# Kernel tuning notes

Measured on AMD Instinct MI355X. Metric: run time of the kernel, lower is better.

The kernel has to match this reference:

```python
import jax, jax.numpy as jnp
import numpy as np

H_IMG, W_IMG = 32, 32   # image_size -> seq_len = 1024
NH, HD, D = 8, 32, 256  # num_heads, head_dim, d_model
B = 8


def _relative_positions(h, w):
    # Swin-style relative position index table, [h*w, h*w] int32
    y = np.arange(h); x = np.arange(w)
    coords = np.stack(np.meshgrid(y, x, indexing='ij')).reshape(2, -1)  # [2, S]
    rel = coords[:, :, None] - coords[:, None, :]                      # [2, S, S]
    rel = rel.transpose(1, 2, 0).astype(np.int64)                      # [S, S, 2]
    rel[:, :, 0] += h - 1
    rel[:, :, 1] += w - 1
    rel[:, :, 0] *= 2 * w - 1
    return np.int32(rel.sum(-1))                                       # [S, S]

_POS = _relative_positions(H_IMG, W_IMG)


def setup_inputs() -> dict:
    key = jax.random.key(0)
    ks = jax.random.split(key, 8)
    S = H_IMG * W_IMG
    return {
        'inputs_q': jax.random.normal(ks[0], (B, S, D), jnp.float32),
        'inputs_kv': jax.random.normal(ks[1], (B, S, D), jnp.float32),
        'Wq': jax.random.normal(ks[2], (D, NH, HD), jnp.float32) / np.sqrt(D),
        'bq': jnp.zeros((NH, HD), jnp.float32),
        'Wk': jax.random.normal(ks[3], (D, NH, HD), jnp.float32) / np.sqrt(D),
        'bk': jnp.zeros((NH, HD), jnp.float32),
        'Wv': jax.random.normal(ks[4], (D, NH, HD), jnp.float32) / np.sqrt(D),
        'bv': jnp.zeros((NH, HD), jnp.float32),
        'rel_table': 0.02 * jax.random.normal(ks[5], ((2 * H_IMG - 1) * (2 * W_IMG - 1), NH), jnp.float32),
        'Wo': jax.random.normal(ks[6], (NH, HD, D), jnp.float32) / np.sqrt(NH * HD),
        'bo': jnp.zeros((D,), jnp.float32),
    }


def reference(inputs_q, inputs_kv, Wq, bq, Wk, bk, Wv, bv, rel_table, Wo, bo):
    pos = jnp.asarray(_POS)                                  # [S, S] int32 (constant)
    q = jnp.einsum('bsd,dhk->bshk', inputs_q, Wq) + bq       # [B, S, H, HD]
    k = jnp.einsum('bsd,dhk->bshk', inputs_kv, Wk) + bk
    v = jnp.einsum('bsd,dhk->bshk', inputs_kv, Wv) + bv
    q = q / jnp.sqrt(jnp.asarray(HD, q.dtype))
    attn = jnp.einsum('bqhd,bkhd->bhqk', q, k)               # [B, H, S, S]
    rel_bias = rel_table[pos]                                # [S, S, H]
    attn = attn + jnp.transpose(rel_bias, (2, 0, 1))[None]   # broadcast over batch
    attn = jax.nn.softmax(attn, axis=-1)
    x = jnp.einsum('bhqk,bkhd->bqhd', attn, v)               # [B, S, H, HD]
    return jnp.einsum('bqhd,hdf->bqf', x, Wo) + bo           # [B, S, D]
```

## Files before the change

### kernel.cpp

```cpp
#include <hip/hip_runtime.h>

#define B_SZ   8
#define S_LEN  1024
#define D_MOD  256
#define NHEADS 8
#define M_ROWS 8192
#define LOG2E  1.4426950408889634f
#define QSCALE_LOG2E 0.2550352766751165f

typedef _Float16 f16x8 __attribute__((ext_vector_type(8)));
typedef _Float16 f16x4 __attribute__((ext_vector_type(4)));
typedef float    f32x4 __attribute__((ext_vector_type(4)));

__global__ __launch_bounds__(256)
void prep_kernel(const float* __restrict__ Wq, const float* __restrict__ Wk,
                 const float* __restrict__ Wv, const float* __restrict__ Wo,
                 const float* __restrict__ rel,
                 _Float16* __restrict__ wtp, _Float16* __restrict__ tab) {
    if (blockIdx.x < 32) {
        __shared__ _Float16 Wl[32 * 264];
        const int mi = blockIdx.x >> 3;
        const int k0 = (blockIdx.x & 7) << 5;
        const float* W = (mi == 0) ? Wq : (mi == 1) ? Wk : (mi == 2) ? Wv : Wo;
        {
            const int r  = threadIdx.x >> 3;
            const int c4 = (threadIdx.x & 7) * 4;
            const float* src = W + (size_t)(k0 + r) * 256 + c4;
#pragma unroll
            for (int g = 0; g < 8; ++g) {
                f32x4 v = *(const f32x4*)(src + g * 32);
                f16x4 o;
#pragma unroll
                for (int j = 0; j < 4; ++j) o[j] = (_Float16)v[j];
                *(f16x4*)(&Wl[r * 264 + c4 + g * 32]) = o;
            }
        }
        __syncthreads();
        const int n16 = threadIdx.x >> 4;
        const int l16 = threadIdx.x & 15;
        const int kk  = k0 >> 5;
#pragma unroll
        for (int quad = 0; quad < 4; ++quad) {
            f16x8 v;
#pragma unroll
            for (int j = 0; j < 8; ++j) v[j] = Wl[(quad * 8 + j) * 264 + n16 * 16 + l16];
            *(f16x8*)(wtp + (((size_t)(mi * 16 + n16) * 8 + kk) << 9) + (quad * 16 + l16) * 8) = v;
        }
        return;
    }
    __shared__ float rl[63 * 8];
    const int dy31 = blockIdx.x - 32;
    for (int f = threadIdx.x; f < 504; f += 256) rl[f] = rel[(size_t)dy31 * 504 + f];
    __syncthreads();
    const int h  = threadIdx.x >> 5;
    const int r5 = threadIdx.x & 31;
#pragma unroll
    for (int c = 0; c < 6; ++c) {
        const int oi   = r5 * 6 + c;
        const int e    = oi >> 6;
        const int lane = oi & 63;
        const int quad = lane >> 4, l16 = lane & 15;
        f16x4 v;
#pragma unroll
        for (int reg = 0; reg < 4; ++reg) {
            const int idx = 16 * e + l16 - quad * 4 - reg + 15;
            v[reg] = (_Float16)(rl[idx * 8 + h] * LOG2E);
        }
        *(f16x4*)(tab + (((size_t)(h * 63 + dy31) * 3 + e) << 8) + lane * 4) = v;
    }
}

__global__ __launch_bounds__(256)
void gemm_qkv_kernel(const float* __restrict__ in_q, const float* __restrict__ in_kv,
                     const _Float16* __restrict__ wtp,
                     const float* __restrict__ bq, const float* __restrict__ bk,
                     const float* __restrict__ bv,
                     _Float16* __restrict__ qs, _Float16* __restrict__ ks,
                     _Float16* __restrict__ vs) {
    __shared__ __align__(16) _Float16 As[64 * 264];
    _Float16* Ta = As;
    _Float16* Tb = As + 64 * 72;

    const int tid  = threadIdx.x;
    const int w    = tid >> 6;
    const int lane = tid & 63;
    const int quad = lane >> 4;
    const int l16  = lane & 15;
    const int m0 = blockIdx.x * 64, n0 = blockIdx.y * 64, z = blockIdx.z;
    const int b = m0 >> 10, mloc = m0 & 1023;

    {
        const int r  = tid >> 2;
        const int c4 = (tid & 3) * 4;
        const float* src = (z ? in_kv : in_q) + (size_t)(m0 + r) * 256 + c4;
        _Float16* dst = As + r * 264 + c4;
#pragma unroll
        for (int g = 0; g < 16; ++g) {
            f32x4 v = *(const f32x4*)(src + g * 16);
            f16x4 o;
#pragma unroll
            for (int j = 0; j < 4; ++j) o[j] = (_Float16)v[j];
            *(f16x4*)(dst + g * 16) = o;
        }
    }
    __syncthreads();

    const int n16base = (n0 >> 4) + (w >> 1) * 2;
    const int mA = z ? 1 : 0;
    const _Float16* wA0 = wtp + (((size_t)(mA * 16 + n16base + 0) * 8) << 9) + lane * 8;
    const _Float16* wA1 = wtp + (((size_t)(mA * 16 + n16base + 1) * 8) << 9) + lane * 8;
    const _Float16* wV0 = wtp + (((size_t)(2 * 16 + n16base + 0) * 8) << 9) + lane * 8;
    const _Float16* wV1 = wtp + (((size_t)(2 * 16 + n16base + 1) * 8) << 9) + lane * 8;
    const _Float16* arow0 = As + ((w & 1) * 32 + l16) * 264;
    const _Float16* arow1 = arow0 + 16 * 264;

    f32x4 accA[2][2], accV[2][2];
#pragma unroll
    for (int i = 0; i < 2; ++i)
#pragma unroll
        for (int j = 0; j < 2; ++j) {
            accA[i][j] = (f32x4){0.f, 0.f, 0.f, 0.f};
            accV[i][j] = (f32x4){0.f, 0.f, 0.f, 0.f};
        }

#pragma unroll
    for (int kk = 0; kk < 8; ++kk) {
        const int k8 = kk * 32 + quad * 8;
        f16x8 a0 = *(const f16x8*)(arow0 + k8);
        f16x8 a1 = *(const f16x8*)(arow1 + k8);
        f16x8 w0 = *(const f16x8*)(wA0 + kk * 512);
        f16x8 w1 = *(const f16x8*)(wA1 + kk * 512);
        accA[0][0] = __builtin_amdgcn_mfma_f32_16x16x32_f16(w0, a0, accA[0][0], 0, 0, 0);
        accA[0][1] = __builtin_amdgcn_mfma_f32_16x16x32_f16(w0, a1, accA[0][1], 0, 0, 0);
        accA[1][0] = __builtin_amdgcn_mfma_f32_16x16x32_f16(w1, a0, accA[1][0], 0, 0, 0);
        accA[1][1] = __builtin_amdgcn_mfma_f32_16x16x32_f16(w1, a1, accA[1][1], 0, 0, 0);
        if (z == 1) {
            f16x8 v0 = *(const f16x8*)(wV0 + kk * 512);
            f16x8 v1 = *(const f16x8*)(wV1 + kk * 512);
            accV[0][0] = __builtin_amdgcn_mfma_f32_16x16x32_f16(a0, v0, accV[0][0], 0, 0, 0);
            accV[0][1] = __builtin_amdgcn_mfma_f32_16x16x32_f16(a0, v1, accV[0][1], 0, 0, 0);
            accV[1][0] = __builtin_amdgcn_mfma_f32_16x16x32_f16(a1, v0, accV[1][0], 0, 0, 0);
            accV[1][1] = __builtin_amdgcn_mfma_f32_16x16x32_f16(a1, v1, accV[1][1], 0, 0, 0);
        }
    }
    __syncthreads();

    {
        const float* biasA = z ? bk : bq;
        const float  sc    = z ? 1.0f : QSCALE_LOG2E;
#pragma unroll
        for (int i = 0; i < 2; ++i) {
            f32x4 b4 = *(const f32x4*)(biasA + n0 + (w >> 1) * 32 + i * 16 + quad * 4);
#pragma unroll
            for (int jj = 0; jj < 2; ++jj) {
                f16x4 pk;
#pragma unroll
                for (int r = 0; r < 4; ++r) pk[r] = (_Float16)((accA[i][jj][r] + b4[r]) * sc);
                *(f16x4*)(Ta + ((w & 1) * 32 + jj * 16 + l16) * 72 +
                               (w >> 1) * 32 + i * 16 + quad * 4) = pk;
            }
        }
        if (z == 1) {
#pragma unroll
            for (int i = 0; i < 2; ++i) {
                const float bvv = bv[n0 + (w >> 1) * 32 + i * 16 + l16];
#pragma unroll
                for (int jj = 0; jj < 2; ++jj) {
                    f16x4 pk;
#pragma unroll
                    for (int r = 0; r < 4; ++r) pk[r] = (_Float16)(accV[jj][i][r] + bvv);
                    *(f16x4*)(Tb + ((w >> 1) * 32 + i * 16 + l16) * 72 +
                                   (w & 1) * 32 + jj * 16 + quad * 4) = pk;
                }
            }
        }
    }
    __syncthreads();
    {
        const int l16c = tid & 15, qdc = (tid >> 4) & 3;
        const int tile0 = mloc >> 5;
#pragma unroll
        for (int c2i = 0; c2i < 2; ++c2i) {
            const int c2 = w * 2 + c2i;
            const int s2 = c2 >> 2, sub = (c2 >> 1) & 1, hs = c2 & 1;
            const int bh = b * 8 + (n0 >> 5) + hs;
            const size_t dbase = (((size_t)(bh * 32 + tile0 + s2) * 2 + sub) << 9) + lane * 8;
            f16x8 va = *(const f16x8*)(Ta + (s2 * 32 + sub * 16 + l16c) * 72 +
                                            hs * 32 + qdc * 8);
            *(f16x8*)((z ? ks : qs) + dbase) = va;
            if (z == 1) {
                f16x8 vb = *(const f16x8*)(Tb + (hs * 32 + sub * 16 + l16c) * 72 +
                                                s2 * 32 + qdc * 8);
                *(f16x8*)(vs + dbase) = vb;
            }
        }
    }
}

__global__ __launch_bounds__(256)
void gemm_out_kernel(const _Float16* __restrict__ xh, const _Float16* __restrict__ wtp,
                     const float* __restrict__ bo, float* __restrict__ out) {
    __shared__ __align__(16) _Float16 As[64 * 264];
    const int tid  = threadIdx.x;
    const int w    = tid >> 6;
    const int lane = tid & 63;
    const int quad = lane >> 4;
    const int l16  = lane & 15;
    const int m0 = blockIdx.x * 64, n0 = blockIdx.y * 64;

    {
        const int r  = tid >> 2;
        const int c8 = (tid & 3) * 8;
        const _Float16* src = xh + (size_t)(m0 + r) * 256 + c8;
        _Float16* dst = As + r * 264 + c8;
#pragma unroll
        for (int g = 0; g < 8; ++g)
            *(f16x8*)(dst + g * 32) = *(const f16x8*)(src + g * 32);
    }
    __syncthreads();

    const int n16base = 48 + (n0 >> 4) + (w >> 1) * 2;
    const _Float16* w0p = wtp + (((size_t)(n16base + 0) * 8) << 9) + lane * 8;
    const _Float16* w1p = wtp + (((size_t)(n16base + 1) * 8) << 9) + lane * 8;
    const _Float16* arow0 = As + ((w & 1) * 32 + l16) * 264;
    const _Float16* arow1 = arow0 + 16 * 264;

    f32x4 acc[2][2];
#pragma unroll
    for (int i = 0; i < 2; ++i)
#pragma unroll
        for (int j = 0; j < 2; ++j) acc[i][j] = (f32x4){0.f, 0.f, 0.f, 0.f};

#pragma unroll
    for (int kk = 0; kk < 8; ++kk) {
        const int k8 = kk * 32 + quad * 8;
        f16x8 a0 = *(const f16x8*)(arow0 + k8);
        f16x8 a1 = *(const f16x8*)(arow1 + k8);
        f16x8 b0 = *(const f16x8*)(w0p + kk * 512);
        f16x8 b1 = *(const f16x8*)(w1p + kk * 512);
        acc[0][0] = __builtin_amdgcn_mfma_f32_16x16x32_f16(a0, b0, acc[0][0], 0, 0, 0);
        acc[0][1] = __builtin_amdgcn_mfma_f32_16x16x32_f16(a0, b1, acc[0][1], 0, 0, 0);
        acc[1][0] = __builtin_amdgcn_mfma_f32_16x16x32_f16(a1, b0, acc[1][0], 0, 0, 0);
        acc[1][1] = __builtin_amdgcn_mfma_f32_16x16x32_f16(a1, b1, acc[1][1], 0, 0, 0);
    }

    __syncthreads();
    {
        float* Tf = (float*)As;
#pragma unroll
        for (int i = 0; i < 2; ++i) {
#pragma unroll
            for (int jj = 0; jj < 2; ++jj) {
#pragma unroll
                for (int r = 0; r < 4; ++r) {
                    const int row = (w & 1) * 32 + jj * 16 + quad * 4 + r;
                    const int col = (w >> 1) * 32 + i * 16 + l16;
                    Tf[row * 68 + col] = acc[jj][i][r];
                }
            }
        }
        __syncthreads();
        const f32x4 bv4 = *(const f32x4*)(bo + n0 + l16 * 4);
#pragma unroll
        for (int g = 0; g < 4; ++g) {
            const int row = w * 16 + g * 4 + quad;
            f32x4 v = *(const f32x4*)(Tf + row * 68 + l16 * 4);
            v += bv4;
            *(f32x4*)(out + (size_t)(m0 + row) * 256 + n0 + l16 * 4) = v;
        }
    }
}

__global__ __launch_bounds__(256)
void attn_kernel(const _Float16* __restrict__ qs, const _Float16* __restrict__ ks,
                 const _Float16* __restrict__ vs, const _Float16* __restrict__ tab,
                 _Float16* __restrict__ xh) {
    __shared__ __align__(16) _Float16 Ps[4][32][40];
    __shared__ __align__(16) _Float16 KVb[2][4][512];

    const int tid  = threadIdx.x;
    const int w    = tid >> 6;
    const int lane = tid & 63;
    const int quad = lane >> 4;
    const int l16  = lane & 15;

    const int n     = blockIdx.x;
    const int xcd   = n & 7;
    const int local = n >> 3;
    const int bh    = xcd * 8 + (local & 7);
    const int qc    = local >> 3;
    const int b = bh >> 3, h = bh & 7;
    const int qrow_base = qc * 128 + w * 32;
    const int yq = qc * 4 + w;

    const _Float16* qp = qs + (((size_t)(bh * 32 + yq) * 2) << 9) + lane * 8;
    const f16x8 qf0 = *(const f16x8*)(qp);
    const f16x8 qf1 = *(const f16x8*)(qp + 512);

    const _Float16* kv = ((w < 2) ? ks : vs) + (((size_t)bh * 64) << 9) +
                         (w & 1) * 512 + lane * 8;
    _Float16* myc0 = &KVb[0][w][lane * 8];
    _Float16* myc1 = &KVb[1][w][lane * 8];

    const _Float16* tb = tab + (((size_t)h * 189) << 8) + lane * 4;

    f16x8 ones;
#pragma unroll
    for (int j = 0; j < 8; ++j) ones[j] = (_Float16)1.0f;

    f32x4 o00 = {0.f,0.f,0.f,0.f}, o01 = {0.f,0.f,0.f,0.f};
    f32x4 o10 = {0.f,0.f,0.f,0.f}, o11 = {0.f,0.f,0.f,0.f};
    f32x4 ol0 = {0.f,0.f,0.f,0.f}, ol1 = {0.f,0.f,0.f,0.f};

    *(f16x8*)myc0 = *(const f16x8*)(kv);
    f32x4 c0, c1, c2;
    {
        const _Float16* t = tb + (yq + 31) * 768;
        f16x4 t0 = *(const f16x4*)(t);
        f16x4 t1 = *(const f16x4*)(t + 256);
        f16x4 t2 = *(const f16x4*)(t + 512);
#pragma unroll
        for (int r = 0; r < 4; ++r) {
            c0[r] = (float)t0[r]; c1[r] = (float)t1[r]; c2[r] = (float)t2[r];
        }
    }
    __syncthreads();

    int cur = 0;
    for (int kt = 0; kt < 32; ++kt) {
        const bool more = (kt < 31);
        f16x8 stg;
        f16x4 n0, n1, n2;
        if (more) {
            stg = *(const f16x8*)(kv + (kt + 1) * 1024);
            const int d = (yq + 30 - kt) * 768;
            n0 = *(const f16x4*)(tb + d);
            n1 = *(const f16x4*)(tb + d + 256);
            n2 = *(const f16x4*)(tb + d + 512);
        }

        const f16x8 kf0 = *(const f16x8*)(&KVb[cur][0][lane * 8]);
        const f16x8 kf1 = *(const f16x8*)(&KVb[cur][1][lane * 8]);
        const f16x8 vf0 = *(const f16x8*)(&KVb[cur][2][lane * 8]);
        const f16x8 vf1 = *(const f16x8*)(&KVb[cur][3][lane * 8]);

        __builtin_amdgcn_s_setprio(1);
        f32x4 s00 = __builtin_amdgcn_mfma_f32_16x16x32_f16(kf0, qf0, c1, 0, 0, 0);
        f32x4 s01 = __builtin_amdgcn_mfma_f32_16x16x32_f16(kf1, qf0, c0, 0, 0, 0);
        f32x4 s10 = __builtin_amdgcn_mfma_f32_16x16x32_f16(kf0, qf1, c2, 0, 0, 0);
        f32x4 s11 = __builtin_amdgcn_mfma_f32_16x16x32_f16(kf1, qf1, c1, 0, 0, 0);
        __builtin_amdgcn_s_setprio(0);

        f16x4 p;
#pragma unroll
        for (int r = 0; r < 4; ++r) p[r] = (_Float16)__builtin_amdgcn_exp2f(s00[r]);
        *(f16x4*)(&Ps[w][l16][quad * 4]) = p;
#pragma unroll
        for (int r = 0; r < 4; ++r) p[r] = (_Float16)__builtin_amdgcn_exp2f(s01[r]);
        *(f16x4*)(&Ps[w][l16][16 + quad * 4]) = p;
#pragma unroll
        for (int r = 0; r < 4; ++r) p[r] = (_Float16)__builtin_amdgcn_exp2f(s10[r]);
        *(f16x4*)(&Ps[w][16 + l16][quad * 4]) = p;
#pragma unroll
        for (int r = 0; r < 4; ++r) p[r] = (_Float16)__builtin_amdgcn_exp2f(s11[r]);
        *(f16x4*)(&Ps[w][16 + l16][16 + quad * 4]) = p;

        const f16x8 pf0 = *(const f16x8*)(&Ps[w][l16][quad * 8]);
        const f16x8 pf1 = *(const f16x8*)(&Ps[w][16 + l16][quad * 8]);
        __builtin_amdgcn_s_setprio(1);
        o00 = __builtin_amdgcn_mfma_f32_16x16x32_f16(vf0, pf0, o00, 0, 0, 0);
        o01 = __builtin_amdgcn_mfma_f32_16x16x32_f16(vf0, pf1, o01, 0, 0, 0);
        o10 = __builtin_amdgcn_mfma_f32_16x16x32_f16(vf1, pf0, o10, 0, 0, 0);
        o11 = __builtin_amdgcn_mfma_f32_16x16x32_f16(vf1, pf1, o11, 0, 0, 0);
        ol0 = __builtin_amdgcn_mfma_f32_16x16x32_f16(ones, pf0, ol0, 0, 0, 0);
        ol1 = __builtin_amdgcn_mfma_f32_16x16x32_f16(ones, pf1, ol1, 0, 0, 0);
        __builtin_amdgcn_s_setprio(0);

        if (more) {
            *(f16x8*)(cur ? myc0 : myc1) = stg;
#pragma unroll
            for (int r = 0; r < 4; ++r) {
                c0[r] = (float)n0[r]; c1[r] = (float)n1[r]; c2[r] = (float)n2[r];
            }
        }
        __syncthreads();
        cur ^= 1;
    }

#pragma unroll
    for (int qh = 0; qh < 2; ++qh) {
        const f32x4 onl = qh ? o01 : o00;
        const f32x4 onh = qh ? o11 : o10;
        const f32x4 ll  = qh ? ol1 : ol0;
        const float inv = __builtin_amdgcn_rcpf(ll[0]);
        const int qg = qrow_base + qh * 16 + l16;
        f16x4 u, v;
#pragma unroll
        for (int r = 0; r < 4; ++r) {
            u[r] = (_Float16)(onl[r] * inv);
            v[r] = (_Float16)(onh[r] * inv);
        }
        _Float16* op = xh + ((size_t)(b * S_LEN + qg)) * D_MOD + h * 32 + quad * 4;
        *(f16x4*)(op)      = u;
        *(f16x4*)(op + 16) = v;
    }
}

extern "C" void kernel_launch(void* const* d_in, const int* in_sizes, int n_in,
                              void* d_out, int out_size, void* d_ws, size_t ws_size,
                              hipStream_t stream) {
    const float* in_q  = (const float*)d_in[0];
    const float* in_kv = (const float*)d_in[1];
    const float* Wq    = (const float*)d_in[2];
    const float* bq    = (const float*)d_in[3];
    const float* Wk    = (const float*)d_in[4];
    const float* bk    = (const float*)d_in[5];
    const float* Wv    = (const float*)d_in[6];
    const float* bv    = (const float*)d_in[7];
    const float* rel   = (const float*)d_in[8];
    const float* Wo    = (const float*)d_in[9];
    const float* bo    = (const float*)d_in[10];
    float* out = (float*)d_out;

    char* wsb = (char*)d_ws;
    _Float16* qs  = (_Float16*)(wsb);
    _Float16* ks  = (_Float16*)(wsb + (size_t)4  * 1048576);
    _Float16* vs  = (_Float16*)(wsb + (size_t)8  * 1048576);
    _Float16* xh  = (_Float16*)(wsb + (size_t)12 * 1048576);
    _Float16* wtp = (_Float16*)(wsb + (size_t)16 * 1048576);
    _Float16* tab = (_Float16*)(wsb + (size_t)17 * 1048576);

    const dim3 blk(256);

    prep_kernel<<<dim3(95), blk, 0, stream>>>(Wq, Wk, Wv, Wo, rel, wtp, tab);
    gemm_qkv_kernel<<<dim3(128, 4, 2), blk, 0, stream>>>(
        in_q, in_kv, wtp, bq, bk, bv, qs, ks, vs);
    attn_kernel<<<dim3(512), blk, 0, stream>>>(qs, ks, vs, tab, xh);
    gemm_out_kernel<<<dim3(128, 4), blk, 0, stream>>>(xh, wtp, bo, out);
}
```

Baseline: 127.1 us.

## Fuse four kernels into one persistent megakernel with atomic grid barriers

Replaces the prep, QKV GEMM, attention and output GEMM launches with a single 512-block kernel whose phases are separated by software grid barriers built on atomic counters. Each block now runs both the Q and KV GEMM passes in a loop instead of using a z grid dimension. The goal is to remove per-launch overhead and the gaps between kernels. In exchange it needs all 512 blocks co-resident (launch_bounds 256,2), adds a memset launch, and spin-wait barrier costs, with deadlock risk if occupancy is not met.

```diff
diff --git a/kernel.cpp b/kernel.cpp
--- a/kernel.cpp
+++ b/kernel.cpp
@@ -12,397 +12,404 @@
 typedef _Float16 f16x4 __attribute__((ext_vector_type(4)));
 typedef float    f32x4 __attribute__((ext_vector_type(4)));
 
-__global__ __launch_bounds__(256)
-void prep_kernel(const float* __restrict__ Wq, const float* __restrict__ Wk,
-                 const float* __restrict__ Wv, const float* __restrict__ Wo,
-                 const float* __restrict__ rel,
-                 _Float16* __restrict__ wtp, _Float16* __restrict__ tab) {
-    if (blockIdx.x < 32) {
-        __shared__ _Float16 Wl[32 * 264];
-        const int mi = blockIdx.x >> 3;
-        const int k0 = (blockIdx.x & 7) << 5;
-        const float* W = (mi == 0) ? Wq : (mi == 1) ? Wk : (mi == 2) ? Wv : Wo;
-        {
-            const int r  = threadIdx.x >> 3;
-            const int c4 = (threadIdx.x & 7) * 4;
-            const float* src = W + (size_t)(k0 + r) * 256 + c4;
-#pragma unroll
-            for (int g = 0; g < 8; ++g) {
-                f32x4 v = *(const f32x4*)(src + g * 32);
-                f16x4 o;
-#pragma unroll
-                for (int j = 0; j < 4; ++j) o[j] = (_Float16)v[j];
-                *(f16x4*)(&Wl[r * 264 + c4 + g * 32]) = o;
-            }
-        }
-        __syncthreads();
-        const int n16 = threadIdx.x >> 4;
-        const int l16 = threadIdx.x & 15;
-        const int kk  = k0 >> 5;
-#pragma unroll
-        for (int quad = 0; quad < 4; ++quad) {
-            f16x8 v;
-#pragma unroll
-            for (int j = 0; j < 8; ++j) v[j] = Wl[(quad * 8 + j) * 264 + n16 * 16 + l16];
-            *(f16x8*)(wtp + (((size_t)(mi * 16 + n16) * 8 + kk) << 9) + (quad * 16 + l16) * 8) = v;
-        }
-        return;
+__device__ __forceinline__ void grid_barrier(int* cnt, int target) {
+    __syncthreads();
+    if (threadIdx.x == 0) {
+        __threadfence();
+        atomicAdd(cnt, 1);
+        while (__hip_atomic_load(cnt, __ATOMIC_ACQUIRE, __HIP_MEMORY_SCOPE_AGENT) < target)
+            __builtin_amdgcn_s_sleep(2);
+        __threadfence();
     }
-    __shared__ float rl[63 * 8];
-    const int dy31 = blockIdx.x - 32;
-    for (int f = threadIdx.x; f < 504; f += 256) rl[f] = rel[(size_t)dy31 * 504 + f];
     __syncthreads();
-    const int h  = threadIdx.x >> 5;
-    const int r5 = threadIdx.x & 31;
-#pragma unroll
-    for (int c = 0; c < 6; ++c) {
-        const int oi   = r5 * 6 + c;
-        const int e    = oi >> 6;
-        const int lane = oi & 63;
-        const int quad = lane >> 4, l16 = lane & 15;
-        f16x4 v;
-#pragma unroll
-        for (int reg = 0; reg < 4; ++reg) {
-            const int idx = 16 * e + l16 - quad * 4 - reg + 15;
-            v[reg] = (_Float16)(rl[idx * 8 + h] * LOG2E);
-        }
-        *(f16x4*)(tab + (((size_t)(h * 63 + dy31) * 3 + e) << 8) + lane * 4) = v;
-    }
 }
 
-__global__ __launch_bounds__(256)
-void gemm_qkv_kernel(const float* __restrict__ in_q, const float* __restrict__ in_kv,
-                     const _Float16* __restrict__ wtp,
-                     const float* __restrict__ bq, const float* __restrict__ bk,
-                     const float* __restrict__ bv,
-                     _Float16* __restrict__ qs, _Float16* __restrict__ ks,
-                     _Float16* __restrict__ vs) {
-    __shared__ __align__(16) _Float16 As[64 * 264];
-    _Float16* Ta = As;
-    _Float16* Tb = As + 64 * 72;
-
+__global__ __launch_bounds__(256, 2)
+void mega_kernel(const float* __restrict__ in_q, const float* __restrict__ in_kv,
+                 const float* __restrict__ Wq, const float* __restrict__ bq,
+                 const float* __restrict__ Wk, const float* __restrict__ bk,
+                 const float* __restrict__ Wv, const float* __restrict__ bv,
+                 const float* __restrict__ rel, const float* __restrict__ Wo,
+                 const float* __restrict__ bo, float* __restrict__ out,
+                 _Float16* __restrict__ qs, _Float16* __restrict__ ks,
+                 _Float16* __restrict__ vs, _Float16* __restrict__ xh,
+                 _Float16* __restrict__ wtp, _Float16* __restrict__ tab,
+                 int* __restrict__ bar) {
+    __shared__ __align__(16) _Float16 SMEM[64 * 264];
+
+    const int bid  = blockIdx.x;
     const int tid  = threadIdx.x;
     const int w    = tid >> 6;
     const int lane = tid & 63;
     const int quad = lane >> 4;
     const int l16  = lane & 15;
-    const int m0 = blockIdx.x * 64, n0 = blockIdx.y * 64, z = blockIdx.z;
-    const int b = m0 >> 10, mloc = m0 & 1023;
+
+    if (bid < 32) {
+        _Float16* Wl = SMEM;
+        const int mi = bid >> 3;
+        const int k0 = (bid & 7) << 5;
+        const float* W = (mi == 0) ? Wq : (mi == 1) ? Wk : (mi == 2) ? Wv : Wo;
+        {
+            const int r  = tid >> 3;
+            const int c4 = (tid & 7) * 4;
+            const float* src = W + (size_t)(k0 + r) * 256 + c4;
+#pragma unroll
+            for (int g = 0; g < 8; ++g) {
+                f32x4 v = *(const f32x4*)(src + g * 32);
+                f16x4 o;
+#pragma unroll
+                for (int j = 0; j < 4; ++j) o[j] = (_Float16)v[j];
+                *(f16x4*)(&Wl[r * 264 + c4 + g * 32]) = o;
+            }
+        }
+        __syncthreads();
+        const int n16 = tid >> 4;
+        const int kk  = k0 >> 5;
+#pragma unroll
+        for (int q2 = 0; q2 < 4; ++q2) {
+            f16x8 v;
+#pragma unroll
+            for (int j = 0; j < 8; ++j) v[j] = Wl[(q2 * 8 + j) * 264 + n16 * 16 + l16];
+            *(f16x8*)(wtp + (((size_t)(mi * 16 + n16) * 8 + kk) << 9) + (q2 * 16 + l16) * 8) = v;
+        }
+    } else if (bid < 95) {
+        float* rl = (float*)SMEM;
+        const int dy31 = bid - 32;
+        for (int f = tid; f < 504; f += 256) rl[f] = rel[(size_t)dy31 * 504 + f];
+        __syncthreads();
+        const int h  = tid >> 5;
+        const int r5 = tid & 31;
+#pragma unroll
+        for (int c = 0; c < 6; ++c) {
+            const int oi   = r5 * 6 + c;
+            const int e    = oi >> 6;
+            const int ln   = oi & 63;
+            const int qd   = ln >> 4, lo = ln & 15;
+            f16x4 v;
+#pragma unroll
+            for (int reg = 0; reg < 4; ++reg) {
+                const int idx = 16 * e + lo - qd * 4 - reg + 15;
+                v[reg] = (_Float16)(rl[idx * 8 + h] * LOG2E);
+            }
+            *(f16x4*)(tab + (((size_t)(h * 63 + dy31) * 3 + e) << 8) + ln * 4) = v;
+        }
+    }
+    grid_barrier(bar + 0, 512);
 
     {
-        const int r  = tid >> 2;
-        const int c4 = (tid & 3) * 4;
-        const float* src = (z ? in_kv : in_q) + (size_t)(m0 + r) * 256 + c4;
-        _Float16* dst = As + r * 264 + c4;
-#pragma unroll
-        for (int g = 0; g < 16; ++g) {
-            f32x4 v = *(const f32x4*)(src + g * 16);
-            f16x4 o;
-#pragma unroll
-            for (int j = 0; j < 4; ++j) o[j] = (_Float16)v[j];
-            *(f16x4*)(dst + g * 16) = o;
+        _Float16* As = SMEM;
+        _Float16* Ta = SMEM;
+        _Float16* Tb = SMEM + 64 * 72;
+        const int m0 = (bid & 127) * 64;
+        const int n0 = ((bid >> 7) & 3) * 64;
+        const int b = m0 >> 10, mloc = m0 & 1023;
+
+        for (int z = 0; z < 2; ++z) {
+            __syncthreads();
+            {
+                const int r  = tid >> 2;
+                const int c4 = (tid & 3) * 4;
+                const float* src = (z ? in_kv : in_q) + (size_t)(m0 + r) * 256 + c4;
+                _Float16* dst = As + r * 264 + c4;
+#pragma unroll
+                for (int g = 0; g < 16; ++g) {
+                    f32x4 v = *(const f32x4*)(src + g * 16);
+                    f16x4 o;
+#pragma unroll
+                    for (int j = 0; j < 4; ++j) o[j] = (_Float16)v[j];
+                    *(f16x4*)(dst + g * 16) = o;
+                }
+            }
+            __syncthreads();
+
+            const int n16base = (n0 >> 4) + (w >> 1) * 2;
+            const int mA = z ? 1 : 0;
+            const _Float16* wA0 = wtp + (((size_t)(mA * 16 + n16base + 0) * 8) << 9) + lane * 8;
+            const _Float16* wA1 = wtp + (((size_t)(mA * 16 + n16base + 1) * 8) << 9) + lane * 8;
+            const _Float16* wV0 = wtp + (((size_t)(2 * 16 + n16base + 0) * 8) << 9) + lane * 8;
+            const _Float16* wV1 = wtp + (((size_t)(2 * 16 + n16base + 1) * 8) << 9) + lane * 8;
+            const _Float16* arow0 = As + ((w & 1) * 32 + l16) * 264;
+            const _Float16* arow1 = arow0 + 16 * 264;
+
+            f32x4 accA[2][2], accV[2][2];
+#pragma unroll
+            for (int i = 0; i < 2; ++i)
+#pragma unroll
+                for (int j = 0; j < 2; ++j) {
+                    accA[i][j] = (f32x4){0.f, 0.f, 0.f, 0.f};
+                    accV[i][j] = (f32x4){0.f, 0.f, 0.f, 0.f};
+                }
+
+#pragma unroll
+            for (int kk = 0; kk < 8; ++kk) {
+                const int k8 = kk * 32 + quad * 8;
+                f16x8 a0 = *(const f16x8*)(arow0 + k8);
+                f16x8 a1 = *(const f16x8*)(arow1 + k8);
+                f16x8 w0 = *(const f16x8*)(wA0 + kk * 512);
+                f16x8 w1 = *(const f16x8*)(wA1 + kk * 512);
+                accA[0][0] = __builtin_amdgcn_mfma_f32_16x16x32_f16(w0, a0, accA[0][0], 0, 0, 0);
+                accA[0][1] = __builtin_amdgcn_mfma_f32_16x16x32_f16(w0, a1, accA[0][1], 0, 0, 0);
+                accA[1][0] = __builtin_amdgcn_mfma_f32_16x16x32_f16(w1, a0, accA[1][0], 0, 0, 0);
+                accA[1][1] = __builtin_amdgcn_mfma_f32_16x16x32_f16(w1, a1, accA[1][1], 0, 0, 0);
+                if (z == 1) {
+                    f16x8 v0 = *(const f16x8*)(wV0 + kk * 512);
+                    f16x8 v1 = *(const f16x8*)(wV1 + kk * 512);
+                    accV[0][0] = __builtin_amdgcn_mfma_f32_16x16x32_f16(a0, v0, accV[0][0], 0, 0, 0);
+                    accV[0][1] = __builtin_amdgcn_mfma_f32_16x16x32_f16(a0, v1, accV[0][1], 0, 0, 0);
+                    accV[1][0] = __builtin_amdgcn_mfma_f32_16x16x32_f16(a1, v0, accV[1][0], 0, 0, 0);
+                    accV[1][1] = __builtin_amdgcn_mfma_f32_16x16x32_f16(a1, v1, accV[1][1], 0, 0, 0);
+                }
+            }
+            __syncthreads();
+
+            {
+                const float* biasA = z ? bk : bq;
+                const float  sc    = z ? 1.0f : QSCALE_LOG2E;
+#pragma unroll
+                for (int i = 0; i < 2; ++i) {
+                    f32x4 b4 = *(const f32x4*)(biasA + n0 + (w >> 1) * 32 + i * 16 + quad * 4);
+#pragma unroll
+                    for (int jj = 0; jj < 2; ++jj) {
+                        f16x4 pk;
+#pragma unroll
+                        for (int r = 0; r < 4; ++r) pk[r] = (_Float16)((accA[i][jj][r] + b4[r]) * sc);
+                        *(f16x4*)(Ta + ((w & 1) * 32 + jj * 16 + l16) * 72 +
+                                       (w >> 1) * 32 + i * 16 + quad * 4) = pk;
+                    }
+                }
+                if (z == 1) {
+#pragma unroll
+                    for (int i = 0; i < 2; ++i) {
+                        const float bvv = bv[n0 + (w >> 1) * 32 + i * 16 + l16];
+#pragma unroll
+                        for (int jj = 0; jj < 2; ++jj) {
+                            f16x4 pk;
+#pragma unroll
+                            for (int r = 0; r < 4; ++r) pk[r] = (_Float16)(accV[jj][i][r] + bvv);
+                            *(f16x4*)(Tb + ((w >> 1) * 32 + i * 16 + l16) * 72 +
+                                           (w & 1) * 32 + jj * 16 + quad * 4) = pk;
+                        }
+                    }
+                }
+            }
+            __syncthreads();
+            {
+                const int l16c = tid & 15, qdc = (tid >> 4) & 3;
+                const int tile0 = mloc >> 5;
+#pragma unroll
+                for (int c2i = 0; c2i < 2; ++c2i) {
+                    const int c2 = w * 2 + c2i;
+                    const int s2 = c2 >> 2, sub = (c2 >> 1) & 1, hs = c2 & 1;
+                    const int bh = b * 8 + (n0 >> 5) + hs;
+                    const size_t dbase = (((size_t)(bh * 32 + tile0 + s2) * 2 + sub) << 9) + lane * 8;
+                    f16x8 va = *(const f16x8*)(Ta + (s2 * 32 + sub * 16 + l16c) * 72 +
+                                                    hs * 32 + qdc * 8);
+                    *(f16x8*)((z ? ks : qs) + dbase) = va;
+                    if (z == 1) {
+                        f16x8 vb = *(const f16x8*)(Tb + (hs * 32 + sub * 16 + l16c) * 72 +
+                                                        s2 * 32 + qdc * 8);
+                        *(f16x8*)(vs + dbase) = vb;
+                    }
+                }
+            }
         }
     }
-    __syncthreads();
-
-    const int n16base = (n0 >> 4) + (w >> 1) * 2;
-    const int mA = z ? 1 : 0;
-    const _Float16* wA0 = wtp + (((size_t)(mA * 16 + n16base + 0) * 8) << 9) + lane * 8;
-    const _Float16* wA1 = wtp + (((size_t)(mA * 16 + n16base + 1) * 8) << 9) + lane * 8;
-    const _Float16* wV0 = wtp + (((size_t)(2 * 16 + n16base + 0) * 8) << 9) + lane * 8;
-    const _Float16* wV1 = wtp + (((size_t)(2 * 16 + n16base + 1) * 8) << 9) + lane * 8;
-    const _Float16* arow0 = As + ((w & 1) * 32 + l16) * 264;
-    const _Float16* arow1 = arow0 + 16 * 264;
-
-    f32x4 accA[2][2], accV[2][2];
-#pragma unroll
-    for (int i = 0; i < 2; ++i)
-#pragma unroll
-        for (int j = 0; j < 2; ++j) {
-            accA[i][j] = (f32x4){0.f, 0.f, 0.f, 0.f};
-            accV[i][j] = (f32x4){0.f, 0.f, 0.f, 0.f};
-        }
-
-#pragma unroll
-    for (int kk = 0; kk < 8; ++kk) {
-        const int k8 = kk * 32 + quad * 8;
-        f16x8 a0 = *(const f16x8*)(arow0 + k8);
-        f16x8 a1 = *(const f16x8*)(arow1 + k8);
-        f16x8 w0 = *(const f16x8*)(wA0 + kk * 512);
-        f16x8 w1 = *(const f16x8*)(wA1 + kk * 512);
-        accA[0][0] = __builtin_amdgcn_mfma_f32_16x16x32_f16(w0, a0, accA[0][0], 0, 0, 0);
-        accA[0][1] = __builtin_amdgcn_mfma_f32_16x16x32_f16(w0, a1, accA[0][1], 0, 0, 0);
-        accA[1][0] = __builtin_amdgcn_mfma_f32_16x16x32_f16(w1, a0, accA[1][0], 0, 0, 0);
-        accA[1][1] = __builtin_amdgcn_mfma_f32_16x16x32_f16(w1, a1, accA[1][1], 0, 0, 0);
-        if (z == 1) {
-            f16x8 v0 = *(const f16x8*)(wV0 + kk * 512);
-            f16x8 v1 = *(const f16x8*)(wV1 + kk * 512);
-            accV[0][0] = __builtin_amdgcn_mfma_f32_16x16x32_f16(a0, v0, accV[0][0], 0, 0, 0);
-            accV[0][1] = __builtin_amdgcn_mfma_f32_16x16x32_f16(a0, v1, accV[0][1], 0, 0, 0);
-            accV[1][0] = __builtin_amdgcn_mfma_f32_16x16x32_f16(a1, v0, accV[1][0], 0, 0, 0);
-            accV[1][1] = __builtin_amdgcn_mfma_f32_16x16x32_f16(a1, v1, accV[1][1], 0, 0, 0);
+    grid_barrier(bar + 1, 512);
+
+    {
+        _Float16* Ps  = SMEM;
+        _Float16* KVb = SMEM + 5120;
+
+        const int xcd   = bid & 7;
+        const int local = bid >> 3;
+        const int bh    = xcd * 8 + (local & 7);
+        const int qc    = local >> 3;
+        const int b = bh >> 3, h = bh & 7;
+        const int qrow_base = qc * 128 + w * 32;
+        const int yq = qc * 4 + w;
+
+        const _Float16* qp = qs + (((size_t)(bh * 32 + yq) * 2) << 9) + lane * 8;
+        const f16x8 qf0 = *(const f16x8*)(qp);
+        const f16x8 qf1 = *(const f16x8*)(qp + 512);
+
+        const _Float16* kv = ((w < 2) ? ks : vs) + (((size_t)bh * 64) << 9) +
+                             (w & 1) * 512 + lane * 8;
+        _Float16* myc0 = KVb + (0 * 4 + w) * 512 + lane * 8;
+        _Float16* myc1 = KVb + (1 * 4 + w) * 512 + lane * 8;
+
+        const _Float16* tb = tab + (((size_t)h * 189) << 8) + lane * 4;
+
+        f16x8 ones;
+#pragma unroll
+        for (int j = 0; j < 8; ++j) ones[j] = (_Float16)1.0f;
+
+        f32x4 o00 = {0.f,0.f,0.f,0.f}, o01 = {0.f,0.f,0.f,0.f};
+        f32x4 o10 = {0.f,0.f,0.f,0.f}, o11 = {0.f,0.f,0.f,0.f};
+        f32x4 ol0 = {0.f,0.f,0.f,0.f}, ol1 = {0.f,0.f,0.f,0.f};
+
+        *(f16x8*)myc0 = *(const f16x8*)(kv);
+        f32x4 c0, c1, c2;
+        {
+            const _Float16* t = tb + (yq + 31) * 768;
+            f16x4 t0 = *(const f16x4*)(t);
+            f16x4 t1 = *(const f16x4*)(t + 256);
+            f16x4 t2 = *(const f16x4*)(t + 512);
+#pragma unroll
+            for (int r = 0; r < 4; ++r) {
+                c0[r] = (float)t0[r]; c1[r] = (float)t1[r]; c2[r] = (float)t2[r];
+            }
+        }
+        __syncthreads();
+
+        int cur = 0;
+        for (int kt = 0; kt < 32; ++kt) {
+            const bool more = (kt < 31);
+            f16x8 stg;
+            f16x4 n0v, n1v, n2v;
+            if (more) {
+                stg = *(const f16x8*)(kv + (kt + 1) * 1024);
+                const int d = (yq + 30 - kt) * 768;
+                n0v = *(const f16x4*)(tb + d);
+                n1v = *(const f16x4*)(tb + d + 256);
+                n2v = *(const f16x4*)(tb + d + 512);
+            }
+
+            const _Float16* kb = KVb + (cur * 4) * 512;
+            const f16x8 kf0 = *(const f16x8*)(kb + 0 * 512 + lane * 8);
+            const f16x8 kf1 = *(const f16x8*)(kb + 1 * 512 + lane * 8);
+            const f16x8 vf0 = *(const f16x8*)(kb + 2 * 512 + lane * 8);
+            const f16x8 vf1 = *(const f16x8*)(kb + 3 * 512 + lane * 8);
+
+            __builtin_amdgcn_s_setprio(1);
+            f32x4 s00 = __builtin_amdgcn_mfma_f32_16x16x32_f16(kf0, qf0, c1, 0, 0, 0);
+            f32x4 s01 = __builtin_amdgcn_mfma_f32_16x16x32_f16(kf1, qf0, c0, 0, 0, 0);
+            f32x4 s10 = __builtin_amdgcn_mfma_f32_16x16x32_f16(kf0, qf1, c2, 0, 0, 0);
+            f32x4 s11 = __builtin_amdgcn_mfma_f32_16x16x32_f16(kf1, qf1, c1, 0, 0, 0);
+            __builtin_amdgcn_s_setprio(0);
+
+            _Float16* pw = Ps + (w * 32) * 40;
+            f16x4 p;
+#pragma unroll
+            for (int r = 0; r < 4; ++r) p[r] = (_Float16)__builtin_amdgcn_exp2f(s00[r]);
+            *(f16x4*)(pw + l16 * 40 + quad * 4) = p;
+#pragma unroll
+            for (int r = 0; r < 4; ++r) p[r] = (_Float16)__builtin_amdgcn_exp2f(s01[r]);
+            *(f16x4*)(pw + l16 * 40 + 16 + quad * 4) = p;
+#pragma unroll
+            for (int r = 0; r < 4; ++r) p[r] = (_Float16)__builtin_amdgcn_exp2f(s10[r]);
+            *(f16x4*)(pw + (16 + l16) * 40 + quad * 4) = p;
+#pragma unroll
+            for (int r = 0; r < 4; ++r) p[r] = (_Float16)__builtin_amdgcn_exp2f(s11[r]);
+            *(f16x4*)(pw + (16 + l16) * 40 + 16 + quad * 4) = p;
+
+            const f16x8 pf0 = *(const f16x8*)(pw + l16 * 40 + quad * 8);
+            const f16x8 pf1 = *(const f16x8*)(pw + (16 + l16) * 40 + quad * 8);
+            __builtin_amdgcn_s_setprio(1);
+            o00 = __builtin_amdgcn_mfma_f32_16x16x32_f16(vf0, pf0, o00, 0, 0, 0);
+            o01 = __builtin_amdgcn_mfma_f32_16x16x32_f16(vf0, pf1, o01, 0, 0, 0);
+            o10 = __builtin_amdgcn_mfma_f32_16x16x32_f16(vf1, pf0, o10, 0, 0, 0);
+            o11 = __builtin_amdgcn_mfma_f32_16x16x32_f16(vf1, pf1, o11, 0, 0, 0);
+            ol0 = __builtin_amdgcn_mfma_f32_16x16x32_f16(ones, pf0, ol0, 0, 0, 0);
+            ol1 = __builtin_amdgcn_mfma_f32_16x16x32_f16(ones, pf1, ol1, 0, 0, 0);
+            __builtin_amdgcn_s_setprio(0);
+
+            if (more) {
+                *(f16x8*)(cur ? myc0 : myc1) = stg;
+#pragma unroll
+                for (int r = 0; r < 4; ++r) {
+                    c0[r] = (float)n0v[r]; c1[r] = (float)n1v[r]; c2[r] = (float)n2v[r];
+                }
+            }
+            __syncthreads();
+            cur ^= 1;
+        }
+
+#pragma unroll
+        for (int qh = 0; qh < 2; ++qh) {
+            const f32x4 onl = qh ? o01 : o00;
+            const f32x4 onh = qh ? o11 : o10;
+            const f32x4 ll  = qh ? ol1 : ol0;
+            const float inv = __builtin_amdgcn_rcpf(ll[0]);
+            const int qg = qrow_base + qh * 16 + l16;
+            f16x4 u, v;
+#pragma unroll
+            for (int r = 0; r < 4; ++r) {
+                u[r] = (_Float16)(onl[r] * inv);
+                v[r] = (_Float16)(onh[r] * inv);
+            }
+            _Float16* op = xh + ((size_t)(b * S_LEN + qg)) * D_MOD + h * 32 + quad * 4;
+            *(f16x4*)(op)      = u;
+            *(f16x4*)(op + 16) = v;
         }
     }
-    __syncthreads();
+    grid_barrier(bar + 2, 512);
 
     {
-        const float* biasA = z ? bk : bq;
-        const float  sc    = z ? 1.0f : QSCALE_LOG2E;
-#pragma unroll
-        for (int i = 0; i < 2; ++i) {
-            f32x4 b4 = *(const f32x4*)(biasA + n0 + (w >> 1) * 32 + i * 16 + quad * 4);
-#pragma unroll
-            for (int jj = 0; jj < 2; ++jj) {
-                f16x4 pk;
-#pragma unroll
-                for (int r = 0; r < 4; ++r) pk[r] = (_Float16)((accA[i][jj][r] + b4[r]) * sc);
-                *(f16x4*)(Ta + ((w & 1) * 32 + jj * 16 + l16) * 72 +
-                               (w >> 1) * 32 + i * 16 + quad * 4) = pk;
-            }
-        }
-        if (z == 1) {
+        _Float16* As = SMEM;
+        const int m0 = (bid & 127) * 64;
+        const int n0 = (bid >> 7) * 64;
+
+        {
+            const int r  = tid >> 2;
+            const int c8 = (tid & 3) * 8;
+            const _Float16* src = xh + (size_t)(m0 + r) * 256 + c8;
+            _Float16* dst = As + r * 264 + c8;
+#pragma unroll
+            for (int g = 0; g < 8; ++g)
+                *(f16x8*)(dst + g * 32) = *(const f16x8*)(src + g * 32);
+        }
+        __syncthreads();
+
+        const int n16base = 48 + (n0 >> 4) + (w >> 1) * 2;
+        const _Float16* w0p = wtp + (((size_t)(n16base + 0) * 8) << 9) + lane * 8;
+        const _Float16* w1p = wtp + (((size_t)(n16base + 1) * 8) << 9) + lane * 8;
+        const _Float16* arow0 = As + ((w & 1) * 32 + l16) * 264;
+        const _Float16* arow1 = arow0 + 16 * 264;
+
+        f32x4 acc[2][2];
+#pragma unroll
+        for (int i = 0; i < 2; ++i)
+#pragma unroll
+            for (int j = 0; j < 2; ++j) acc[i][j] = (f32x4){0.f, 0.f, 0.f, 0.f};
+
+#pragma unroll
+        for (int kk = 0; kk < 8; ++kk) {
+            const int k8 = kk * 32 + quad * 8;
+            f16x8 a0 = *(const f16x8*)(arow0 + k8);
+            f16x8 a1 = *(const f16x8*)(arow1 + k8);
+            f16x8 b0 = *(const f16x8*)(w0p + kk * 512);
+            f16x8 b1 = *(const f16x8*)(w1p + kk * 512);
+            acc[0][0] = __builtin_amdgcn_mfma_f32_16x16x32_f16(a0, b0, acc[0][0], 0, 0, 0);
+            acc[0][1] = __builtin_amdgcn_mfma_f32_16x16x32_f16(a0, b1, acc[0][1], 0, 0, 0);
+            acc[1][0] = __builtin_amdgcn_mfma_f32_16x16x32_f16(a1, b0, acc[1][0], 0, 0, 0);
+            acc[1][1] = __builtin_amdgcn_mfma_f32_16x16x32_f16(a1, b1, acc[1][1], 0, 0, 0);
+        }
+
+        __syncthreads();
+        {
+            float* Tf = (float*)As;
 #pragma unroll
             for (int i = 0; i < 2; ++i) {
-                const float bvv = bv[n0 + (w >> 1) * 32 + i * 16 + l16];
 #pragma unroll
                 for (int jj = 0; jj < 2; ++jj) {
-                    f16x4 pk;
-#pragma unroll
-                    for (int r = 0; r < 4; ++r) pk[r] = (_Float16)(accV[jj][i][r] + bvv);
-                    *(f16x4*)(Tb + ((w >> 1) * 32 + i * 16 + l16) * 72 +
-                                   (w & 1) * 32 + jj * 16 + quad * 4) = pk;
-                }
-            }
-        }
-    }
-    __syncthreads();
-    {
-        const int l16c = tid & 15, qdc = (tid >> 4) & 3;
-        const int tile0 = mloc >> 5;
-#pragma unroll
-        for (int c2i = 0; c2i < 2; ++c2i) {
-            const int c2 = w * 2 + c2i;
-            const int s2 = c2 >> 2, sub = (c2 >> 1) & 1, hs = c2 & 1;
-            const int bh = b * 8 + (n0 >> 5) + hs;
-            const size_t dbase = (((size_t)(bh * 32 + tile0 + s2) * 2 + sub) << 9) + lane * 8;
-            f16x8 va = *(const f16x8*)(Ta + (s2 * 32 + sub * 16 + l16c) * 72 +
-                                            hs * 32 + qdc * 8);
-            *(f16x8*)((z ? ks : qs) + dbase) = va;
-            if (z == 1) {
-                f16x8 vb = *(const f16x8*)(Tb + (hs * 32 + sub * 16 + l16c) * 72 +
-                                                s2 * 32 + qdc * 8);
-                *(f16x8*)(vs + dbase) = vb;
-            }
-        }
-    }
-}
-
-__global__ __launch_bounds__(256)
-void gemm_out_kernel(const _Float16* __restrict__ xh, const _Float16* __restrict__ wtp,
-                     const float* __restrict__ bo, float* __restrict__ out) {
-    __shared__ __align__(16) _Float16 As[64 * 264];
-    const int tid  = threadIdx.x;
-    const int w    = tid >> 6;
-    const int lane = tid & 63;
-    const int quad = lane >> 4;
-    const int l16  = lane & 15;
-    const int m0 = blockIdx.x * 64, n0 = blockIdx.y * 64;
-
-    {
-        const int r  = tid >> 2;
-        const int c8 = (tid & 3) * 8;
-        const _Float16* src = xh + (size_t)(m0 + r) * 256 + c8;
-        _Float16* dst = As + r * 264 + c8;
-#pragma unroll
-        for (int g = 0; g < 8; ++g)
-            *(f16x8*)(dst + g * 32) = *(const f16x8*)(src + g * 32);
-    }
-    __syncthreads();
-
-    const int n16base = 48 + (n0 >> 4) + (w >> 1) * 2;
-    const _Float16* w0p = wtp + (((size_t)(n16base + 0) * 8) << 9) + lane * 8;
-    const _Float16* w1p = wtp + (((size_t)(n16base + 1) * 8) << 9) + lane * 8;
-    const _Float16* arow0 = As + ((w & 1) * 32 + l16) * 264;
-    const _Float16* arow1 = arow0 + 16 * 264;
-
-    f32x4 acc[2][2];
-#pragma unroll
-    for (int i = 0; i < 2; ++i)
-#pragma unroll
-        for (int j = 0; j < 2; ++j) acc[i][j] = (f32x4){0.f, 0.f, 0.f, 0.f};
-
-#pragma unroll
-    for (int kk = 0; kk < 8; ++kk) {
-        const int k8 = kk * 32 + quad * 8;
-        f16x8 a0 = *(const f16x8*)(arow0 + k8);
-        f16x8 a1 = *(const f16x8*)(arow1 + k8);
-        f16x8 b0 = *(const f16x8*)(w0p + kk * 512);
-        f16x8 b1 = *(const f16x8*)(w1p + kk * 512);
-        acc[0][0] = __builtin_amdgcn_mfma_f32_16x16x32_f16(a0, b0, acc[0][0], 0, 0, 0);
-        acc[0][1] = __builtin_amdgcn_mfma_f32_16x16x32_f16(a0, b1, acc[0][1], 0, 0, 0);
-        acc[1][0] = __builtin_amdgcn_mfma_f32_16x16x32_f16(a1, b0, acc[1][0], 0, 0, 0);
-        acc[1][1] = __builtin_amdgcn_mfma_f32_16x16x32_f16(a1, b1, acc[1][1], 0, 0, 0);
-    }
-
-    __syncthreads();
-    {
-        float* Tf = (float*)As;
-#pragma unroll
-        for (int i = 0; i < 2; ++i) {
-#pragma unroll
-            for (int jj = 0; jj < 2; ++jj) {
-#pragma unroll
-                for (int r = 0; r < 4; ++r) {
-                    const int row = (w & 1) * 32 + jj * 16 + quad * 4 + r;
-                    const int col = (w >> 1) * 32 + i * 16 + l16;
-                    Tf[row * 68 + col] = acc[jj][i][r];
-                }
-            }
-        }
-        __syncthreads();
-        const f32x4 bv4 = *(const f32x4*)(bo + n0 + l16 * 4);
-#pragma unroll
-        for (int g = 0; g < 4; ++g) {
-            const int row = w * 16 + g * 4 + quad;
-            f32x4 v = *(const f32x4*)(Tf + row * 68 + l16 * 4);
-            v += bv4;
-            *(f32x4*)(out + (size_t)(m0 + row) * 256 + n0 + l16 * 4) = v;
-        }
-    }
-}
-
-__global__ __launch_bounds__(256)
-void attn_kernel(const _Float16* __restrict__ qs, const _Float16* __restrict__ ks,
-                 const _Float16* __restrict__ vs, const _Float16* __restrict__ tab,
-                 _Float16* __restrict__ xh) {
-    __shared__ __align__(16) _Float16 Ps[4][32][40];
-    __shared__ __align__(16) _Float16 KVb[2][4][512];
-
-    const int tid  = threadIdx.x;
-    const int w    = tid >> 6;
-    const int lane = tid & 63;
-    const int quad = lane >> 4;
-    const int l16  = lane & 15;
-
-    const int n     = blockIdx.x;
-    const int xcd   = n & 7;
-    const int local = n >> 3;
-    const int bh    = xcd * 8 + (local & 7);
-    const int qc    = local >> 3;
-    const int b = bh >> 3, h = bh & 7;
-    const int qrow_base = qc * 128 + w * 32;
-    const int yq = qc * 4 + w;
-
-    const _Float16* qp = qs + (((size_t)(bh * 32 + yq) * 2) << 9) + lane * 8;
-    const f16x8 qf0 = *(const f16x8*)(qp);
-    const f16x8 qf1 = *(const f16x8*)(qp + 512);
-
-    const _Float16* kv = ((w < 2) ? ks : vs) + (((size_t)bh * 64) << 9) +
-                         (w & 1) * 512 + lane * 8;
-    _Float16* myc0 = &KVb[0][w][lane * 8];
-    _Float16* myc1 = &KVb[1][w][lane * 8];
-
-    const _Float16* tb = tab + (((size_t)h * 189) << 8) + lane * 4;
-
-    f16x8 ones;
-#pragma unroll
-    for (int j = 0; j < 8; ++j) ones[j] = (_Float16)1.0f;
-
-    f32x4 o00 = {0.f,0.f,0.f,0.f}, o01 = {0.f,0.f,0.f,0.f};
-    f32x4 o10 = {0.f,0.f,0.f,0.f}, o11 = {0.f,0.f,0.f,0.f};
-    f32x4 ol0 = {0.f,0.f,0.f,0.f}, ol1 = {0.f,0.f,0.f,0.f};
-
-    *(f16x8*)myc0 = *(const f16x8*)(kv);
-    f32x4 c0, c1, c2;
-    {
-        const _Float16* t = tb + (yq + 31) * 768;
-        f16x4 t0 = *(const f16x4*)(t);
-        f16x4 t1 = *(const f16x4*)(t + 256);
-        f16x4 t2 = *(const f16x4*)(t + 512);
-#pragma unroll
-        for (int r = 0; r < 4; ++r) {
-            c0[r] = (float)t0[r]; c1[r] = (float)t1[r]; c2[r] = (float)t2[r];
-        }
-    }
-    __syncthreads();
-
-    int cur = 0;
-    for (int kt = 0; kt < 32; ++kt) {
-        const bool more = (kt < 31);
-        f16x8 stg;
-        f16x4 n0, n1, n2;
-        if (more) {
-            stg = *(const f16x8*)(kv + (kt + 1) * 1024);
-            const int d = (yq + 30 - kt) * 768;
-            n0 = *(const f16x4*)(tb + d);
-            n1 = *(const f16x4*)(tb + d + 256);
-            n2 = *(const f16x4*)(tb + d + 512);
-        }
-
-        const f16x8 kf0 = *(const f16x8*)(&KVb[cur][0][lane * 8]);
-        const f16x8 kf1 = *(const f16x8*)(&KVb[cur][1][lane * 8]);
-        const f16x8 vf0 = *(const f16x8*)(&KVb[cur][2][lane * 8]);
-        const f16x8 vf1 = *(const f16x8*)(&KVb[cur][3][lane * 8]);
-
-        __builtin_amdgcn_s_setprio(1);
-        f32x4 s00 = __builtin_amdgcn_mfma_f32_16x16x32_f16(kf0, qf0, c1, 0, 0, 0);
-        f32x4 s01 = __builtin_amdgcn_mfma_f32_16x16x32_f16(kf1, qf0, c0, 0, 0, 0);
-        f32x4 s10 = __builtin_amdgcn_mfma_f32_16x16x32_f16(kf0, qf1, c2, 0, 0, 0);
-        f32x4 s11 = __builtin_amdgcn_mfma_f32_16x16x32_f16(kf1, qf1, c1, 0, 0, 0);
-        __builtin_amdgcn_s_setprio(0);
-
-        f16x4 p;
-#pragma unroll
-        for (int r = 0; r < 4; ++r) p[r] = (_Float16)__builtin_amdgcn_exp2f(s00[r]);
-        *(f16x4*)(&Ps[w][l16][quad * 4]) = p;
-#pragma unroll
-        for (int r = 0; r < 4; ++r) p[r] = (_Float16)__builtin_amdgcn_exp2f(s01[r]);
-        *(f16x4*)(&Ps[w][l16][16 + quad * 4]) = p;
-#pragma unroll
-        for (int r = 0; r < 4; ++r) p[r] = (_Float16)__builtin_amdgcn_exp2f(s10[r]);
-        *(f16x4*)(&Ps[w][16 + l16][quad * 4]) = p;
-#pragma unroll
-        for (int r = 0; r < 4; ++r) p[r] = (_Float16)__builtin_amdgcn_exp2f(s11[r]);
-        *(f16x4*)(&Ps[w][16 + l16][16 + quad * 4]) = p;
-
-        const f16x8 pf0 = *(const f16x8*)(&Ps[w][l16][quad * 8]);
-        const f16x8 pf1 = *(const f16x8*)(&Ps[w][16 + l16][quad * 8]);
-        __builtin_amdgcn_s_setprio(1);
-        o00 = __builtin_amdgcn_mfma_f32_16x16x32_f16(vf0, pf0, o00, 0, 0, 0);
-        o01 = __builtin_amdgcn_mfma_f32_16x16x32_f16(vf0, pf1, o01, 0, 0, 0);
-        o10 = __builtin_amdgcn_mfma_f32_16x16x32_f16(vf1, pf0, o10, 0, 0, 0);
-        o11 = __builtin_amdgcn_mfma_f32_16x16x32_f16(vf1, pf1, o11, 0, 0, 0);
-        ol0 = __builtin_amdgcn_mfma_f32_16x16x32_f16(ones, pf0, ol0, 0, 0, 0);
-        ol1 = __builtin_amdgcn_mfma_f32_16x16x32_f16(ones, pf1, ol1, 0, 0, 0);
-        __builtin_amdgcn_s_setprio(0);
-
-        if (more) {
-            *(f16x8*)(cur ? myc0 : myc1) = stg;
-#pragma unroll
-            for (int r = 0; r < 4; ++r) {
-                c0[r] = (float)n0[r]; c1[r] = (float)n1[r]; c2[r] = (float)n2[r];
-            }
-        }
-        __syncthreads();
-        cur ^= 1;
-    }
-
-#pragma unroll
-    for (int qh = 0; qh < 2; ++qh) {
-        const f32x4 onl = qh ? o01 : o00;
-        const f32x4 onh = qh ? o11 : o10;
-        const f32x4 ll  = qh ? ol1 : ol0;
-        const float inv = __builtin_amdgcn_rcpf(ll[0]);
-        const int qg = qrow_base + qh * 16 + l16;
-        f16x4 u, v;
-#pragma unroll
-        for (int r = 0; r < 4; ++r) {
-            u[r] = (_Float16)(onl[r] * inv);
-            v[r] = (_Float16)(onh[r] * inv);
-        }
-        _Float16* op = xh + ((size_t)(b * S_LEN + qg)) * D_MOD + h * 32 + quad * 4;
-        *(f16x4*)(op)      = u;
-        *(f16x4*)(op + 16) = v;
+#pragma unroll
+                    for (int r = 0; r < 4; ++r) {
+                        const int row = (w & 1) * 32 + jj * 16 + quad * 4 + r;
+                        const int col = (w >> 1) * 32 + i * 16 + l16;
+                        Tf[row * 68 + col] = acc[jj][i][r];
+                    }
+                }
+            }
+            __syncthreads();
+            const f32x4 bv4 = *(const f32x4*)(bo + n0 + l16 * 4);
+#pragma unroll
+            for (int g = 0; g < 4; ++g) {
+                const int row = w * 16 + g * 4 + quad;
+                f32x4 v = *(const f32x4*)(Tf + row * 68 + l16 * 4);
+                v += bv4;
+                *(f32x4*)(out + (size_t)(m0 + row) * 256 + n0 + l16 * 4) = v;
+            }
+        }
     }
 }
 
@@ -429,12 +436,10 @@
     _Float16* xh  = (_Float16*)(wsb + (size_t)12 * 1048576);
     _Float16* wtp = (_Float16*)(wsb + (size_t)16 * 1048576);
     _Float16* tab = (_Float16*)(wsb + (size_t)17 * 1048576);
-
-    const dim3 blk(256);
-
-    prep_kernel<<<dim3(95), blk, 0, stream>>>(Wq, Wk, Wv, Wo, rel, wtp, tab);
-    gemm_qkv_kernel<<<dim3(128, 4, 2), blk, 0, stream>>>(
-        in_q, in_kv, wtp, bq, bk, bv, qs, ks, vs);
-    attn_kernel<<<dim3(512), blk, 0, stream>>>(qs, ks, vs, tab, xh);
-    gemm_out_kernel<<<dim3(128, 4), blk, 0, stream>>>(xh, wtp, bo, out);
+    int*      bar = (int*)     (wsb + (size_t)19 * 1048576);
+
+    hipMemsetAsync(bar, 0, 3 * sizeof(int), stream);
+    mega_kernel<<<dim3(512), dim3(256), 0, stream>>>(
+        in_q, in_kv, Wq, bq, Wk, bk, Wv, bv, rel, Wo, bo, out,
+        qs, ks, vs, xh, wtp, tab, bar);
 }
```

After: 319.8 us. 2.52x slower.
